# Optimization experiments

Hardware: AMD Instinct MI355X
Metric: run time of the kernel (lower is better)

Reference implementation:

```python
import jax, jax.numpy as jnp
import numpy as np

DIM = 1024
NUM_HEADS = 16
HEAD_DIM = DIM // NUM_HEADS
THETA = 10000.0


def apply_rope(x):
    # x: [B, S, H, D]; Llama-style interleaved rotary pairs.
    S, D = x.shape[1], x.shape[3]
    half = D // 2
    inv_freq = THETA ** (-jnp.arange(half, dtype=jnp.float32) * 2.0 / D)  # [D/2]
    angles = jnp.arange(S, dtype=jnp.float32)[:, None] * inv_freq[None, :]  # [S, D/2]
    cos = jnp.cos(angles)[None, :, None, :]  # [1,S,1,D/2]
    sin = jnp.sin(angles)[None, :, None, :]
    x_even = x[..., 0::2]
    x_odd = x[..., 1::2]
    out_even = x_even * cos - x_odd * sin
    out_odd = x_even * sin + x_odd * cos
    out = jnp.stack([out_even, out_odd], axis=-1).reshape(x.shape)
    return out.astype(x.dtype)


def setup_inputs() -> dict:
    key = jax.random.key(0)
    ks = jax.random.split(key, 5)
    B, S = 2, 2048
    x = jax.random.normal(ks[0], (B, S, DIM), dtype=jnp.float32)
    scale = 1.0 / np.sqrt(DIM)
    Wq = jax.random.normal(ks[1], (DIM, DIM), dtype=jnp.float32) * scale
    Wk = jax.random.normal(ks[2], (DIM, DIM), dtype=jnp.float32) * scale
    Wv = jax.random.normal(ks[3], (DIM, DIM), dtype=jnp.float32) * scale
    Wo = jax.random.normal(ks[4], (DIM, DIM), dtype=jnp.float32) * scale
    return {"x": x, "Wq": Wq, "Wk": Wk, "Wv": Wv, "Wo": Wo}


def reference(x, Wq, Wk, Wv, Wo):
    B, S, _ = x.shape
    # torch Linear: y = x @ W^T
    q = (x @ Wq.T).reshape(B, S, NUM_HEADS, HEAD_DIM)
    k = (x @ Wk.T).reshape(B, S, NUM_HEADS, HEAD_DIM)
    v = (x @ Wv.T).reshape(B, S, NUM_HEADS, HEAD_DIM)
    q = apply_rope(q)
    k = apply_rope(k)
    # causal SDPA, scale = 1/sqrt(head_dim)
    scale = 1.0 / np.sqrt(HEAD_DIM).astype(np.float32)
    scores = jnp.einsum("bqhd,bkhd->bhqk", q, k) * scale  # [B,H,S,S]
    causal = jnp.tril(jnp.ones((S, S), dtype=bool))
    scores = jnp.where(causal[None, None], scores, jnp.finfo(scores.dtype).min)
    attn = jax.nn.softmax(scores, axis=-1)
    y = jnp.einsum("bhqk,bkhd->bqhd", attn, v).reshape(B, S, DIM)
    return y @ Wo.T
```

## Files before the change

kernel.cpp:

```cpp
#include <hip/hip_runtime.h>
#include <hip/hip_bf16.h>

typedef __attribute__((ext_vector_type(8))) __bf16 bf16x8;
typedef __attribute__((ext_vector_type(4))) __bf16 bf16x4;
typedef __attribute__((ext_vector_type(4))) float f32x4;
typedef __attribute__((ext_vector_type(16))) float f32x16;
typedef __attribute__((ext_vector_type(2))) unsigned int uint2v;
typedef __attribute__((ext_vector_type(4))) unsigned int uint4v;

#define DIM 1024
#define SLEN 2048
#define NH 16
#define HD 64

__device__ __forceinline__ f32x4 MFMA(bf16x8 a, bf16x8 b, f32x4 c) {
    return __builtin_amdgcn_mfma_f32_16x16x32_bf16(a, b, c, 0, 0, 0);
}
__device__ __forceinline__ f32x16 MFMA32(bf16x8 a, bf16x8 b, f32x16 c) {
    return __builtin_amdgcn_mfma_f32_32x32x16_bf16(a, b, c, 0, 0, 0);
}
__device__ __forceinline__ unsigned pack_bf16(float a, float b) {
    unsigned short ua = __builtin_bit_cast(unsigned short, (__bf16)a);
    unsigned short ub = __builtin_bit_cast(unsigned short, (__bf16)b);
    return ((unsigned)ub << 16) | (unsigned)ua;
}

__global__ __launch_bounds__(256) void cvt_bf16(const float* __restrict__ in,
                                                __bf16* __restrict__ out, int n) {
    int i = (blockIdx.x * blockDim.x + threadIdx.x) * 8;
    if (i >= n) return;
    f32x4 a = *reinterpret_cast<const f32x4*>(in + i);
    f32x4 b = *reinterpret_cast<const f32x4*>(in + i + 4);
    bf16x8 o;
#pragma unroll
    for (int j = 0; j < 4; ++j) { o[j] = (__bf16)a[j]; o[j + 4] = (__bf16)b[j]; }
    *reinterpret_cast<bf16x8*>(out + i) = o;
}

__global__ __launch_bounds__(256) void cvt_w4(const float* __restrict__ w0,
                                              const float* __restrict__ w1,
                                              const float* __restrict__ w2,
                                              const float* __restrict__ w3,
                                              __bf16* __restrict__ o0,
                                              __bf16* __restrict__ o1,
                                              __bf16* __restrict__ o2,
                                              __bf16* __restrict__ o3) {
    int s = blockIdx.y;
    const float* in = s == 0 ? w0 : s == 1 ? w1 : s == 2 ? w2 : w3;
    __bf16* out = s == 0 ? o0 : s == 1 ? o1 : s == 2 ? o2 : o3;
    int i = (blockIdx.x * blockDim.x + threadIdx.x) * 8;
    f32x4 a = *reinterpret_cast<const f32x4*>(in + i);
    f32x4 b = *reinterpret_cast<const f32x4*>(in + i + 4);
    bf16x8 o;
#pragma unroll
    for (int j = 0; j < 4; ++j) { o[j] = (__bf16)a[j]; o[j + 4] = (__bf16)b[j]; }
    *reinterpret_cast<bf16x8*>(out + i) = o;
}

__global__ __launch_bounds__(256) void rope2(__bf16* __restrict__ q,
                                             __bf16* __restrict__ k) {
    __bf16* t = blockIdx.y == 0 ? q : k;
    const float scale = blockIdx.y == 0 ? 0.18033688011112042f : 1.0f;
    int idx = blockIdx.x * blockDim.x + threadIdx.x;
    int row = idx >> 9;
    int p = idx & 511;
    int head = p >> 5;
    int j = p & 31;
    int s = row & (SLEN - 1);
    float inv = expf(-0.28782313662425574f * (float)j);
    float angle = (float)s * inv;
    float sn, cs;
    sincosf(angle, &sn, &cs);
    size_t base = (size_t)row * DIM + head * HD + 2 * j;
    float e = (float)t[base], o = (float)t[base + 1];
    t[base] = (__bf16)((e * cs - o * sn) * scale);
    t[base + 1] = (__bf16)((e * sn + o * cs) * scale);
}

__global__ __launch_bounds__(256) void gemm_qkv(const __bf16* __restrict__ X,
                                                const __bf16* __restrict__ Wq,
                                                const __bf16* __restrict__ Wk,
                                                const __bf16* __restrict__ Wv,
                                                __bf16* __restrict__ Qo,
                                                __bf16* __restrict__ Ko,
                                                __bf16* __restrict__ Vt) {
    __shared__ alignas(16) __bf16 Alds[128 * 64];
    __shared__ alignas(16) __bf16 Blds[128 * 64];
    const int tid = threadIdx.x;
    const int lane = tid & 63;
    const int w = tid >> 6;
    const int wr = w >> 1, wc = w & 1;
    const int l15 = lane & 15, lhi = lane >> 4;
    const int l7 = l15 & 7;
    const int m0 = blockIdx.y * 128;
    const int n0g = blockIdx.x * 128;
    const int seg = n0g >> 10;
    const int n0 = n0g & 1023;
    const __bf16* __restrict__ B = seg == 0 ? Wq : seg == 1 ? Wk : Wv;
    const int K = 1024, N = 1024;

    const int lrow = lane >> 3;
    const int scol = ((lane & 7) ^ lrow) * 8;

    f32x4 acc[4][4] = {};

    for (int kt = 0; kt < K; kt += 64) {
#pragma unroll
        for (int c = 0; c < 4; ++c) {
            int r0 = c * 32 + w * 8;
            const __bf16* sa = &X[(size_t)(m0 + r0 + lrow) * K + kt + scol];
            const __bf16* sb = &B[(size_t)(n0 + r0 + lrow) * K + kt + scol];
            __builtin_amdgcn_global_load_lds((const __attribute__((address_space(1))) void*)sa,
                                             (__attribute__((address_space(3))) void*)&Alds[r0 * 64],
                                             16, 0, 0);
            __builtin_amdgcn_global_load_lds((const __attribute__((address_space(1))) void*)sb,
                                             (__attribute__((address_space(3))) void*)&Blds[r0 * 64],
                                             16, 0, 0);
        }
        __syncthreads();
#pragma unroll
        for (int kk = 0; kk < 2; ++kk) {
            bf16x8 af[4], bfr[4];
#pragma unroll
            for (int i = 0; i < 4; ++i) {
                af[i] = *(const bf16x8*)&Alds[(wr * 64 + i * 16 + l15) * 64 + 8 * ((kk * 4 + lhi) ^ l7)];
                bfr[i] = *(const bf16x8*)&Blds[(wc * 64 + i * 16 + l15) * 64 + 8 * ((kk * 4 + lhi) ^ l7)];
            }
            __builtin_amdgcn_s_setprio(1);
#pragma unroll
            for (int i = 0; i < 4; ++i)
#pragma unroll
                for (int j = 0; j < 4; ++j)
                    acc[i][j] = MFMA(af[i], bfr[j], acc[i][j]);
            __builtin_amdgcn_s_setprio(0);
        }
        __syncthreads();
    }
    if (seg < 2) {
        __bf16* __restrict__ O = seg == 0 ? Qo : Ko;
#pragma unroll
        for (int i = 0; i < 4; ++i)
#pragma unroll
            for (int j = 0; j < 4; ++j)
#pragma unroll
                for (int r = 0; r < 4; ++r) {
                    int row = m0 + wr * 64 + i * 16 + lhi * 4 + r;
                    int col = n0 + wc * 64 + j * 16 + l15;
                    O[(size_t)row * N + col] = (__bf16)acc[i][j][r];
                }
    } else {
#pragma unroll
        for (int i = 0; i < 4; ++i)
#pragma unroll
            for (int j = 0; j < 4; ++j) {
                int row = m0 + wr * 64 + i * 16 + lhi * 4;
                int col = n0 + wc * 64 + j * 16 + l15;
                int bb = row >> 11, s = row & 2047;
                int hh = col >> 6, d = col & 63;
                bf16x4 pk;
#pragma unroll
                for (int r = 0; r < 4; ++r) pk[r] = (__bf16)acc[i][j][r];
                *(bf16x4*)&Vt[((size_t)(bb * 16 + hh) * 64 + d) * SLEN + s] = pk;
            }
    }
}

__global__ __launch_bounds__(256) void gemm_o(const __bf16* __restrict__ A,
                                              const __bf16* __restrict__ B,
                                              float* __restrict__ C) {
    __shared__ alignas(16) __bf16 Alds[64 * 64];
    __shared__ alignas(16) __bf16 Blds[128 * 64];
    const int tid = threadIdx.x;
    const int lane = tid & 63;
    const int w = tid >> 6;
    const int wr = w >> 1, wc = w & 1;
    const int l15 = lane & 15, lhi = lane >> 4;
    const int l7 = l15 & 7;
    const int m0 = blockIdx.y * 64;
    const int n0 = blockIdx.x * 128;
    const int K = 1024, N = 1024;

    const int lrow = lane >> 3;
    const int scol = ((lane & 7) ^ lrow) * 8;

    f32x4 acc[2][4] = {};

    for (int kt = 0; kt < K; kt += 64) {
#pragma unroll
        for (int c = 0; c < 2; ++c) {
            int r0 = c * 32 + w * 8;
            const __bf16* sa = &A[(size_t)(m0 + r0 + lrow) * K + kt + scol];
            __builtin_amdgcn_global_load_lds((const __attribute__((address_space(1))) void*)sa,
                                             (__attribute__((address_space(3))) void*)&Alds[r0 * 64],
                                             16, 0, 0);
        }
#pragma unroll
        for (int c = 0; c < 4; ++c) {
            int r0 = c * 32 + w * 8;
            const __bf16* sb = &B[(size_t)(n0 + r0 + lrow) * K + kt + scol];
            __builtin_amdgcn_global_load_lds((const __attribute__((address_space(1))) void*)sb,
                                             (__attribute__((address_space(3))) void*)&Blds[r0 * 64],
                                             16, 0, 0);
        }
        __syncthreads();
#pragma unroll
        for (int kk = 0; kk < 2; ++kk) {
            bf16x8 af[2], bfr[4];
#pragma unroll
            for (int i = 0; i < 2; ++i)
                af[i] = *(const bf16x8*)&Alds[(wr * 32 + i * 16 + l15) * 64 + 8 * ((kk * 4 + lhi) ^ l7)];
#pragma unroll
            for (int j = 0; j < 4; ++j)
                bfr[j] = *(const bf16x8*)&Blds[(wc * 64 + j * 16 + l15) * 64 + 8 * ((kk * 4 + lhi) ^ l7)];
            __builtin_amdgcn_s_setprio(1);
#pragma unroll
            for (int i = 0; i < 2; ++i)
#pragma unroll
                for (int j = 0; j < 4; ++j)
                    acc[i][j] = MFMA(af[i], bfr[j], acc[i][j]);
            __builtin_amdgcn_s_setprio(0);
        }
        __syncthreads();
    }
#pragma unroll
    for (int i = 0; i < 2; ++i)
#pragma unroll
        for (int j = 0; j < 4; ++j)
#pragma unroll
            for (int r = 0; r < 4; ++r) {
                int row = m0 + wr * 32 + i * 16 + lhi * 4 + r;
                int col = n0 + wc * 64 + j * 16 + l15;
                C[(size_t)row * N + col] = acc[i][j][r];
            }
}

__global__ __launch_bounds__(256, 4) void attn_kernel(const __bf16* __restrict__ Q,
                                                      const __bf16* __restrict__ K,
                                                      const __bf16* __restrict__ Vt,
                                                      __bf16* __restrict__ Y) {
    __shared__ __bf16 Klds[2][64 * 64];
    __shared__ __bf16 Vlds[2][64 * 64];

    const int tid = threadIdx.x;
    const int lane = tid & 63;
    const int w = tid >> 6;
    const int qhalf = w & 1, khalf = w >> 1;
    const int l31 = lane & 31;
    const int hi32 = lane >> 5;
    const int l7 = l31 & 7;

    const int id = blockIdx.x;
    const int x = id & 7, jj = id >> 3;
    const int qi = jj >> 2;
    const int g = qi >> 3, r = qi & 7;
    const int qt = g == 0 ? 31 - r : g == 1 ? r : g == 2 ? 23 - r : 8 + r;
    const int bh = 4 * x + (jj & 3);
    const int b = bh >> 4, h = bh & 15;

    const int srow = lane >> 3;
    const int scs = (lane & 7) ^ srow;
    const __bf16* skP = K + (size_t)b * SLEN * DIM + h * HD + (size_t)(8 * w + srow) * DIM + scs * 8;
    const __bf16* svP = Vt + (size_t)bh * 64 * SLEN + (size_t)(8 * w + srow) * SLEN + scs * 8;
    const int dA = (8 * w + srow) * 64;

    auto stage = [&](int buf) {
#pragma unroll
        for (int i = 0; i < 2; ++i) {
            __builtin_amdgcn_global_load_lds(
                (const __attribute__((address_space(1))) void*)(skP + (size_t)i * 32 * DIM),
                (__attribute__((address_space(3))) void*)&Klds[buf][dA + i * 32 * 64], 16, 0, 0);
            __builtin_amdgcn_global_load_lds(
                (const __attribute__((address_space(1))) void*)(svP + (size_t)i * 32 * SLEN),
                (__attribute__((address_space(3))) void*)&Vlds[buf][dA + i * 32 * 64], 16, 0, 0);
        }
        skP += 64 * DIM;
        svP += 64;
    };

    const int qloc = qhalf * 32 + l31;
    const int qg = qt * 64 + qloc;
    const size_t qbase = (size_t)(b * SLEN + qg) * DIM + h * HD;
    bf16x8 qf0 = *(const bf16x8*)&Q[qbase + 0 + 8 * hi32];
    bf16x8 qf1 = *(const bf16x8*)&Q[qbase + 16 + 8 * hi32];
    bf16x8 qf2 = *(const bf16x8*)&Q[qbase + 32 + 8 * hi32];
    bf16x8 qf3 = *(const bf16x8*)&Q[qbase + 48 + 8 * hi32];

    const int krowbase = (khalf * 32 + l31) * 64;
    const int koff0 = krowbase + 8 * ((0 + hi32) ^ l7);
    const int koff1 = krowbase + 8 * ((2 + hi32) ^ l7);
    const int koff2 = krowbase + 8 * ((4 + hi32) ^ l7);
    const int koff3 = krowbase + 8 * ((6 + hi32) ^ l7);
    const int vrow0 = l31 * 64, vrow1 = (32 + l31) * 64;
    const int voff00 = vrow0 + 8 * ((4 * khalf + 0 + hi32) ^ l7);
    const int voff01 = vrow0 + 8 * ((4 * khalf + 2 + hi32) ^ l7);
    const int voff10 = vrow1 + 8 * ((4 * khalf + 0 + hi32) ^ l7);
    const int voff11 = vrow1 + 8 * ((4 * khalf + 2 + hi32) ^ l7);

    bf16x8 ones;
#pragma unroll
    for (int t = 0; t < 8; ++t) ones[t] = (__bf16)1.0f;

    f32x16 acc0 = {}, acc1 = {};
    f32x16 accL = {};

    const int nkt = qt + 1;
    stage(0);
    for (int kt = 0; kt < nkt; ++kt) {
        const int cur = kt & 1;
        __syncthreads();
        if (kt + 1 < nkt) stage(cur ^ 1);
        const __bf16* Kc = Klds[cur];
        const __bf16* Vc = Vlds[cur];

        f32x16 S = {};
        __builtin_amdgcn_s_setprio(1);
        S = MFMA32(*(const bf16x8*)&Kc[koff0], qf0, S);
        S = MFMA32(*(const bf16x8*)&Kc[koff1], qf1, S);
        S = MFMA32(*(const bf16x8*)&Kc[koff2], qf2, S);
        S = MFMA32(*(const bf16x8*)&Kc[koff3], qf3, S);
        __builtin_amdgcn_s_setprio(0);

        if (kt == qt) {
#pragma unroll
            for (int r2 = 0; r2 < 16; ++r2) {
                const int krow = (r2 & 3) + 8 * (r2 >> 2) + 4 * hi32 + 32 * khalf;
                if (krow > qloc) S[r2] = -1e30f;
            }
        }
        float p[16];
#pragma unroll
        for (int r2 = 0; r2 < 16; ++r2) p[r2] = exp2f(S[r2] - 16.0f);

        bf16x8 pf[2];
#pragma unroll
        for (int ss = 0; ss < 2; ++ss) {
            unsigned P01 = pack_bf16(p[8 * ss + 0], p[8 * ss + 1]);
            unsigned P23 = pack_bf16(p[8 * ss + 2], p[8 * ss + 3]);
            unsigned Q01 = pack_bf16(p[8 * ss + 4], p[8 * ss + 5]);
            unsigned Q23 = pack_bf16(p[8 * ss + 6], p[8 * ss + 7]);
            uint2v sa = __builtin_amdgcn_permlane32_swap(P01, Q01, false, false);
            uint2v sb = __builtin_amdgcn_permlane32_swap(P23, Q23, false, false);
            uint4v pwv = {sa[0], sb[0], sa[1], sb[1]};
            pf[ss] = __builtin_bit_cast(bf16x8, pwv);
        }

        __builtin_amdgcn_s_setprio(1);
        accL = MFMA32(ones, pf[0], accL);
        accL = MFMA32(ones, pf[1], accL);
        acc0 = MFMA32(*(const bf16x8*)&Vc[voff00], pf[0], acc0);
        acc0 = MFMA32(*(const bf16x8*)&Vc[voff01], pf[1], acc0);
        acc1 = MFMA32(*(const bf16x8*)&Vc[voff10], pf[0], acc1);
        acc1 = MFMA32(*(const bf16x8*)&Vc[voff11], pf[1], acc1);
        __builtin_amdgcn_s_setprio(0);
    }

    float lsum = accL[0];
    float* fbuf = (float*)&Klds[0][0];
    float* lbuf = (float*)&Vlds[0][0];
    __syncthreads();
    if (khalf == 1) {
#pragma unroll
        for (int r2 = 0; r2 < 16; ++r2) {
            fbuf[(qhalf * 2 + 0) * 1024 + r2 * 64 + lane] = acc0[r2];
            fbuf[(qhalf * 2 + 1) * 1024 + r2 * 64 + lane] = acc1[r2];
        }
        lbuf[qhalf * 64 + lane] = lsum;
    }
    __syncthreads();
    if (khalf == 0) {
#pragma unroll
        for (int r2 = 0; r2 < 16; ++r2) {
            acc0[r2] += fbuf[(qhalf * 2 + 0) * 1024 + r2 * 64 + lane];
            acc1[r2] += fbuf[(qhalf * 2 + 1) * 1024 + r2 * 64 + lane];
        }
        lsum += lbuf[qhalf * 64 + lane];
        const float inv = 1.0f / lsum;
        const size_t obase = (size_t)(b * SLEN + qg) * DIM + h * HD;
#pragma unroll
        for (int gg = 0; gg < 4; ++gg) {
            bf16x4 o0, o1;
#pragma unroll
            for (int e = 0; e < 4; ++e) {
                o0[e] = (__bf16)(acc0[gg * 4 + e] * inv);
                o1[e] = (__bf16)(acc1[gg * 4 + e] * inv);
            }
            *(bf16x4*)&Y[obase + 8 * gg + 4 * hi32] = o0;
            *(bf16x4*)&Y[obase + 32 + 8 * gg + 4 * hi32] = o1;
        }
    }
}

extern "C" void kernel_launch(void* const* d_in, const int* in_sizes, int n_in,
                              void* d_out, int out_size, void* d_ws, size_t ws_size,
                              hipStream_t stream) {
    const float* x = (const float*)d_in[0];
    const float* Wq = (const float*)d_in[1];
    const float* Wk = (const float*)d_in[2];
    const float* Wv = (const float*)d_in[3];
    const float* Wo = (const float*)d_in[4];
    float* out = (float*)d_out;

    const size_t XN = (size_t)4096 * 1024;
    const size_t WN = (size_t)1024 * 1024;

    __bf16* xb = (__bf16*)d_ws;
    __bf16* qb = xb + XN;
    __bf16* kb = qb + XN;
    __bf16* vtb = kb + XN;
    __bf16* wqb = vtb + XN;
    __bf16* wkb = wqb + WN;
    __bf16* wvb = wkb + WN;
    __bf16* wob = wvb + WN;
    __bf16* yb = xb;

    cvt_bf16<<<XN / 8 / 256, 256, 0, stream>>>(x, xb, (int)XN);
    dim3 gw(WN / 8 / 256, 4);
    cvt_w4<<<gw, 256, 0, stream>>>(Wq, Wk, Wv, Wo, wqb, wkb, wvb, wob);

    dim3 gq(24, 32);
    gemm_qkv<<<gq, 256, 0, stream>>>(xb, wqb, wkb, wvb, qb, kb, vtb);

    int pairs = 4096 * (DIM / 2);
    dim3 gr(pairs / 256, 2);
    rope2<<<gr, 256, 0, stream>>>(qb, kb);

    attn_kernel<<<1024, 256, 0, stream>>>(qb, kb, vtb, yb);

    dim3 go(8, 64);
    gemm_o<<<go, 256, 0, stream>>>(yb, wob, out);
}
```

Baseline: 110.3 us.

## Triple-buffer K/V tiles in attention with explicit vmcnt waits and longest-first ordering

The attention kernel's K/V LDS staging moves from double to triple buffering, prefetching two tiles ahead. A manual s_waitcnt vmcnt plus raw s_barrier replaces __syncthreads, so loads for later tiles stay in flight. The query-tile schedule becomes a simple longest-first order instead of the interleaved one. LDS use rises by half, so occupancy drops (launch bounds 4 to 3 blocks), and the hand-tuned vmcnt count depends on the exact number of loads per stage.

```diff
diff --git a/kernel.cpp b/kernel.cpp
--- a/kernel.cpp
+++ b/kernel.cpp
@@ -234,12 +234,12 @@
             }
 }
 
-__global__ __launch_bounds__(256, 4) void attn_kernel(const __bf16* __restrict__ Q,
+__global__ __launch_bounds__(256, 3) void attn_kernel(const __bf16* __restrict__ Q,
                                                       const __bf16* __restrict__ K,
                                                       const __bf16* __restrict__ Vt,
                                                       __bf16* __restrict__ Y) {
-    __shared__ __bf16 Klds[2][64 * 64];
-    __shared__ __bf16 Vlds[2][64 * 64];
+    __shared__ __bf16 Kb[3 * 64 * 64];
+    __shared__ __bf16 Vb[3 * 64 * 64];
 
     const int tid = threadIdx.x;
     const int lane = tid & 63;
@@ -251,9 +251,7 @@
 
     const int id = blockIdx.x;
     const int x = id & 7, jj = id >> 3;
-    const int qi = jj >> 2;
-    const int g = qi >> 3, r = qi & 7;
-    const int qt = g == 0 ? 31 - r : g == 1 ? r : g == 2 ? 23 - r : 8 + r;
+    const int qt = 31 - (jj >> 2);
     const int bh = 4 * x + (jj & 3);
     const int b = bh >> 4, h = bh & 15;
 
@@ -268,10 +266,10 @@
         for (int i = 0; i < 2; ++i) {
             __builtin_amdgcn_global_load_lds(
                 (const __attribute__((address_space(1))) void*)(skP + (size_t)i * 32 * DIM),
-                (__attribute__((address_space(3))) void*)&Klds[buf][dA + i * 32 * 64], 16, 0, 0);
+                (__attribute__((address_space(3))) void*)&Kb[buf * 4096 + dA + i * 32 * 64], 16, 0, 0);
             __builtin_amdgcn_global_load_lds(
                 (const __attribute__((address_space(1))) void*)(svP + (size_t)i * 32 * SLEN),
-                (__attribute__((address_space(3))) void*)&Vlds[buf][dA + i * 32 * 64], 16, 0, 0);
+                (__attribute__((address_space(3))) void*)&Vb[buf * 4096 + dA + i * 32 * 64], 16, 0, 0);
         }
         skP += 64 * DIM;
         svP += 64;
@@ -305,12 +303,23 @@
 
     const int nkt = qt + 1;
     stage(0);
+    if (nkt > 1) stage(1);
+    int cur = 0, sbuf = 2;
     for (int kt = 0; kt < nkt; ++kt) {
-        const int cur = kt & 1;
-        __syncthreads();
-        if (kt + 1 < nkt) stage(cur ^ 1);
-        const __bf16* Kc = Klds[cur];
-        const __bf16* Vc = Vlds[cur];
+        if (kt < nkt - 1) {
+            asm volatile("s_waitcnt vmcnt(4)" ::: "memory");
+        } else {
+            asm volatile("s_waitcnt vmcnt(0)" ::: "memory");
+        }
+        __builtin_amdgcn_s_barrier();
+        __builtin_amdgcn_sched_barrier(0);
+        if (kt + 2 < nkt) {
+            stage(sbuf);
+            sbuf = sbuf == 2 ? 0 : sbuf + 1;
+        }
+        const __bf16* Kc = &Kb[cur * 4096];
+        const __bf16* Vc = &Vb[cur * 4096];
+        cur = cur == 2 ? 0 : cur + 1;
 
         f32x16 S = {};
         __builtin_amdgcn_s_setprio(1);
@@ -355,8 +364,8 @@
     }
 
     float lsum = accL[0];
-    float* fbuf = (float*)&Klds[0][0];
-    float* lbuf = (float*)&Vlds[0][0];
+    float* fbuf = (float*)&Kb[0];
+    float* lbuf = (float*)&Vb[0];
     __syncthreads();
     if (khalf == 1) {
 #pragma unroll
```

Measured after the change: 110.3 us. About the same (+0.0%).
